# Optimization experiments

Hardware: AMD Instinct MI355X
Metric: run time of the kernel (lower is better)

## Reference

```python
import jax, jax.numpy as jnp
import numpy as np

B, S, I, H, C = 512, 128, 64, 256, 10


def setup_inputs() -> dict:
    key = jax.random.key(0)
    ks = jax.random.split(key, 9)
    u = lambda k, shape, lo, hi: jax.random.uniform(k, shape, jnp.float32, lo, hi)
    return {
        "x": jax.random.normal(ks[0], (B, S, I), jnp.float32),
        # LTCCell params (uniform init per init_parameters)
        "W_gd": u(ks[1], (2 * H, I + H), -0.1, 0.1),
        "b_gd": u(ks[2], (2 * H,), -0.1, 0.1),
        "W_tau": u(ks[3], (H, H), -0.1, 0.1),
        "b_tau": u(ks[4], (H,), -0.1, 0.1),
        "gleak": u(ks[5], (H,), 0.001, 1.0),
        "cm": u(ks[6], (H,), 0.4, 0.6),
        # classifier head
        "W_fc": jax.random.normal(ks[7], (C, H), jnp.float32) * 0.05,
        "b_fc": jax.random.normal(ks[8], (C,), jnp.float32) * 0.05,
    }


def reference(x, W_gd, b_gd, W_tau, b_tau, gleak, cm, W_fc, b_fc):
    # Constant part of the denominator (elementwise, hidden_dim)
    const_den = jax.nn.softplus(cm) + jax.nn.softplus(gleak)  # [H]

    def dhdt(h, x_t):
        # LTCCell.forward: dh/dt
        combined = jnp.concatenate([x_t, h], axis=1)          # [B, I+H]
        gd = combined @ W_gd.T + b_gd                          # [B, 2H]
        gate, dyn = jnp.split(gd, 2, axis=1)
        tau = jax.nn.softplus(h @ W_tau.T + b_tau)             # [B, H]
        num = jax.nn.sigmoid(gate) * jnp.tanh(dyn) - h
        return num / (tau + const_den + 1e-6)

    def step(h, x_t):
        # torchdiffeq 'rk4' fixed-grid = 3/8-rule RK4, single step dt=1 over [0,1]
        k1 = dhdt(h, x_t)
        k2 = dhdt(h + k1 / 3.0, x_t)
        k3 = dhdt(h + (k2 - k1 / 3.0), x_t)
        k4 = dhdt(h + (k1 - k2 + k3), x_t)
        h_new = h + (k1 + 3.0 * (k2 + k3) + k4) * 0.125
        return h_new, None

    h0 = jnp.zeros((x.shape[0], H), x.dtype)
    xs = jnp.transpose(x, (1, 0, 2))                           # [S, B, I]
    h_final, _ = jax.lax.scan(step, h0, xs)
    return h_final @ W_fc.T + b_fc                             # [B, C]
```

## Files before the change

kernel.cpp:

```cpp
#include <hip/hip_runtime.h>

typedef __attribute__((ext_vector_type(8))) short bf16x8;
typedef __attribute__((ext_vector_type(4))) float f32x4;
typedef __attribute__((ext_vector_type(2))) _Float16 f16x2;

#define MFMA(a, b, c) __builtin_amdgcn_mfma_f32_16x16x32_bf16((a), (b), (c), 0, 0, 0)

__device__ __forceinline__ unsigned short f2bf(float f) {
    unsigned int u = __builtin_bit_cast(unsigned int, f);
    return (unsigned short)((u + 0x7FFFu + ((u >> 16) & 1u)) >> 16);
}

__global__ __launch_bounds__(256) void prepack_kernel(const float* __restrict__ W_gd,
                                                      unsigned short* __restrict__ ws) {
    int i = blockIdx.x * 256 + threadIdx.x;
    ws[i] = f2bf(W_gd[(256 + (i >> 8)) * 320 + 64 + (i & 255)]);
    if (i < 32768) ws[65536 + i] = f2bf(W_gd[(i >> 6) * 320 + (i & 63)]);
}

__global__ __launch_bounds__(512, 1)
void ltc_kernel(
    const float* __restrict__ x, const float* __restrict__ W_gd,
    const float* __restrict__ b_gd, const float* __restrict__ W_tau,
    const float* __restrict__ b_tau, const float* __restrict__ gleak,
    const float* __restrict__ cm, const float* __restrict__ W_fc,
    const float* __restrict__ b_fc, const unsigned short* __restrict__ ws,
    float* __restrict__ out)
{
    const int tid  = threadIdx.x;
    const int lane = tid & 63;
    const int wv   = tid >> 6;
    const int c16  = lane & 15;
    const int kg   = lane >> 4;
    const int row0 = blockIdx.x * 2;

    __shared__ __align__(16) unsigned short tauL[65536];
    __shared__ __align__(16) unsigned short dynL[8192];
    __shared__ __align__(16) unsigned short abuf[2][264];
    __shared__ __align__(16) unsigned short xbuf[2][72];
    __shared__ float hout[2][257];

    const int uA = 32 * wv + c16;
    const int uB = uA + 16;
    const int swzA = (uA & 7) << 3;
    const int swzD = (uA & 3) << 3;

    for (int i = tid; i < 65536; i += 512) {
        int u = i >> 8, k = i & 255;
        tauL[u * 256 + (k ^ ((u & 7) << 3))] = f2bf(W_tau[u * 256 + k]);
    }
    for (int i = tid; i < 8192; i += 512) {
        int u = i >> 5, k = i & 31;
        dynL[u * 32 + (k ^ ((u & 3) << 3))] = f2bf(W_gd[(256 + u) * 320 + 64 + k]);
    }
    for (int i = tid; i < 2 * 264; i += 512) ((unsigned short*)abuf)[i] = 0;

    bf16x8 Wg[2][8];
    {
        const int wrow[2] = { uA, uB };
        #pragma unroll
        for (int t = 0; t < 2; ++t) {
            const float* src = W_gd + wrow[t] * 320 + 64;
            #pragma unroll
            for (int s = 0; s < 8; ++s) {
                const float4* p = (const float4*)(src + s * 32 + kg * 8);
                float4 a = p[0], b = p[1];
                bf16x8 v;
                v[0] = (short)f2bf(a.x); v[1] = (short)f2bf(a.y);
                v[2] = (short)f2bf(a.z); v[3] = (short)f2bf(a.w);
                v[4] = (short)f2bf(b.x); v[5] = (short)f2bf(b.y);
                v[6] = (short)f2bf(b.z); v[7] = (short)f2bf(b.w);
                Wg[t][s] = v;
            }
        }
    }

    const float btau0 = b_tau[uA], btau1 = b_tau[uB];
    const float cden0 = __logf(1.f + __expf(cm[uA])) + __logf(1.f + __expf(gleak[uA])) + 1e-6f;
    const float cden1 = __logf(1.f + __expf(cm[uB])) + __logf(1.f + __expf(gleak[uB])) + 1e-6f;
    float bgd[4] = { b_gd[uA], b_gd[uB], b_gd[256 + uA], b_gd[256 + uB] };

    const int rsel = (c16 < 2) ? c16 : 0;
    const unsigned short* aptr = &abuf[rsel][kg * 8];
    const unsigned short* xptr = &xbuf[rsel][kg * 8];
    const unsigned short* wsx  = ws + 65536;

    float hv[2][2] = {{0.f, 0.f}, {0.f, 0.f}};
    f16x2 zh; zh[0] = (_Float16)0.f; zh[1] = (_Float16)0.f;
    f16x2 kk1[2] = { zh, zh }, kk2[2] = { zh, zh }, kk3[2] = { zh, zh };

    __syncthreads();

    #pragma unroll 1
    for (int ts = 0; ts < 128; ++ts) {
        if (tid < 128) {
            int r = tid >> 6, i = tid & 63;
            xbuf[r][i] = f2bf(x[((row0 + r) * 128 + ts) * 64 + i]);
        }
        __syncthreads();

        f32x4 gx[4];
        #pragma unroll
        for (int t = 0; t < 4; ++t) gx[t] = (f32x4){0.f, 0.f, 0.f, 0.f};
        {
            const int xo[4] = { uA, uB, 256 + uA, 256 + uB };
            #pragma unroll
            for (int s = 0; s < 2; ++s) {
                bf16x8 ax = *(const bf16x8*)(xptr + s * 32);
                #pragma unroll
                for (int t = 0; t < 4; ++t) {
                    bf16x8 bx = *(const bf16x8*)(wsx + xo[t] * 64 + s * 32 + kg * 8);
                    gx[t] = MFMA(ax, bx, gx[t]);
                }
            }
        }
        f16x2 gdx[4];
        #pragma unroll
        for (int t = 0; t < 4; ++t) {
            gdx[t][0] = (_Float16)(gx[t][0] + bgd[t]);
            gdx[t][1] = (_Float16)(gx[t][1] + bgd[t]);
        }

        #pragma unroll
        for (int stg = 0; stg < 4; ++stg) {
            f32x4 T0 = {0.f,0.f,0.f,0.f}, T1 = {0.f,0.f,0.f,0.f};
            f32x4 G0 = {0.f,0.f,0.f,0.f}, G1 = {0.f,0.f,0.f,0.f};
            #pragma unroll
            for (int s = 0; s < 8; ++s) {
                bf16x8 A  = *(const bf16x8*)(aptr + s * 32);
                bf16x8 tA = *(const bf16x8*)(tauL + uA * 256 + ((s * 32 + kg * 8) ^ swzA));
                bf16x8 tB = *(const bf16x8*)(tauL + uB * 256 + ((s * 32 + kg * 8) ^ swzA));
                T0 = MFMA(A, tA, T0);
                T1 = MFMA(A, tB, T1);
                G0 = MFMA(A, Wg[0][s], G0);
                G1 = MFMA(A, Wg[1][s], G1);
            }
            float den[2][2];
            den[0][0] = __logf(1.f + __expf(T0[0] + btau0)) + cden0;
            den[0][1] = __logf(1.f + __expf(T0[1] + btau0)) + cden0;
            den[1][0] = __logf(1.f + __expf(T1[0] + btau1)) + cden1;
            den[1][1] = __logf(1.f + __expf(T1[1] + btau1)) + cden1;

            f32x4 D0 = {0.f,0.f,0.f,0.f};
            {
                bf16x8 A0 = *(const bf16x8*)(aptr);
                bf16x8 dA = *(const bf16x8*)(dynL + uA * 32 + ((kg * 8) ^ swzD));
                D0 = MFMA(A0, dA, D0);
                #pragma unroll
                for (int s = 1; s < 8; ++s) {
                    bf16x8 A = *(const bf16x8*)(aptr + s * 32);
                    bf16x8 B = *(const bf16x8*)(ws + uA * 256 + s * 32 + kg * 8);
                    D0 = MFMA(A, B, D0);
                }
            }
            f32x4 D1 = {0.f,0.f,0.f,0.f};
            {
                bf16x8 A0 = *(const bf16x8*)(aptr);
                bf16x8 dB = *(const bf16x8*)(dynL + uB * 32 + ((kg * 8) ^ swzD));
                D1 = MFMA(A0, dB, D1);
                #pragma unroll
                for (int s = 1; s < 8; ++s) {
                    bf16x8 A = *(const bf16x8*)(aptr + s * 32);
                    bf16x8 B = *(const bf16x8*)(ws + uB * 256 + s * 32 + kg * 8);
                    D1 = MFMA(A, B, D1);
                }
            }
            __syncthreads();

            #pragma unroll
            for (int ti = 0; ti < 2; ++ti) {
                #pragma unroll
                for (int r = 0; r < 2; ++r) {
                    float gate = (ti == 0 ? G0[r] : G1[r]) + (float)gdx[ti][r];
                    float dyn  = (ti == 0 ? D0[r] : D1[r]) + (float)gdx[2 + ti][r];
                    float sig = __fdividef(1.f, 1.f + __expf(-gate));
                    float th  = 1.f - __fdividef(2.f, __expf(2.f * dyn) + 1.f);
                    float k1v = (float)kk1[ti][r];
                    float k2v = (float)kk2[ti][r];
                    float k3v = (float)kk3[ti][r];
                    float h0 = hv[ti][r];
                    float ec;
                    if      (stg == 0) ec = h0;
                    else if (stg == 1) ec = h0 + k1v * (1.f / 3.f);
                    else if (stg == 2) ec = h0 - k1v * (1.f / 3.f) + k2v;
                    else               ec = h0 + k1v - k2v + k3v;
                    float kv = __fdividef(sig * th - ec, den[ti][r]);
                    float en;
                    if (stg == 0)      { kk1[ti][r] = (_Float16)kv; en = h0 + kv * (1.f / 3.f); }
                    else if (stg == 1) { kk2[ti][r] = (_Float16)kv; en = h0 - k1v * (1.f / 3.f) + kv; }
                    else if (stg == 2) { kk3[ti][r] = (_Float16)kv; en = h0 + k1v - k2v + kv; }
                    else               { en = h0 + 0.125f * (k1v + 3.f * (k2v + k3v) + kv); hv[ti][r] = en; }
                    if (lane < 16) {
                        int u = (ti == 0) ? uA : uB;
                        abuf[r][u] = f2bf(en);
                    }
                }
            }
            __syncthreads();
        }
    }

    if (lane < 16) {
        hout[0][uA] = hv[0][0]; hout[1][uA] = hv[0][1];
        hout[0][uB] = hv[1][0]; hout[1][uB] = hv[1][1];
    }
    __syncthreads();
    if (tid < 20) {
        int r = tid / 10, c = tid % 10;
        float acc = b_fc[c];
        for (int k = 0; k < 256; ++k) acc = fmaf(hout[r][k], W_fc[c * 256 + k], acc);
        out[(row0 + r) * 10 + c] = acc;
    }
}

extern "C" void kernel_launch(void* const* d_in, const int* in_sizes, int n_in,
                              void* d_out, int out_size, void* d_ws, size_t ws_size,
                              hipStream_t stream) {
    (void)in_sizes; (void)n_in; (void)out_size; (void)ws_size;
    unsigned short* ws16 = (unsigned short*)d_ws;
    prepack_kernel<<<256, 256, 0, stream>>>((const float*)d_in[1], ws16);
    ltc_kernel<<<256, 512, 0, stream>>>(
        (const float*)d_in[0], (const float*)d_in[1], (const float*)d_in[2],
        (const float*)d_in[3], (const float*)d_in[4], (const float*)d_in[5],
        (const float*)d_in[6], (const float*)d_in[7], (const float*)d_in[8],
        ws16, (float*)d_out);
}
```

Measured before the change: 1.130 ms.

## Software-pipeline global dyn-weight loads and split per-unit MFMA chains with elementwise overlap

Restructures each RK stage so the tau, gate and dyn MFMA chains for unit A are computed and their elementwise update done before unit B's chains. This lets unit B's matrix work overlap unit A's transcendental math. Global loads of the dyn weights are software-pipelined through a rotating 4-entry register buffer so each load is issued several MFMAs before use. The tau LDS swizzle is widened to 16 rows, and the bias and constant denominators move into shared memory to free registers. The cost is more complex index bookkeeping in the rotating buffer, with possible register pressure or scheduling changes.

```diff
diff --git a/kernel.cpp b/kernel.cpp
--- a/kernel.cpp
+++ b/kernel.cpp
@@ -9,6 +9,9 @@
 __device__ __forceinline__ unsigned short f2bf(float f) {
     unsigned int u = __builtin_bit_cast(unsigned int, f);
     return (unsigned short)((u + 0x7FFFu + ((u >> 16) & 1u)) >> 16);
+}
+__device__ __forceinline__ float softplusf(float v) {
+    return __logf(1.f + __expf(v));
 }
 
 __global__ __launch_bounds__(256) void prepack_kernel(const float* __restrict__ W_gd,
@@ -32,28 +35,42 @@
     const int wv   = tid >> 6;
     const int c16  = lane & 15;
     const int kg   = lane >> 4;
+    const int kg8  = kg * 8;
     const int row0 = blockIdx.x * 2;
 
     __shared__ __align__(16) unsigned short tauL[65536];
     __shared__ __align__(16) unsigned short dynL[8192];
     __shared__ __align__(16) unsigned short abuf[2][264];
     __shared__ __align__(16) unsigned short xbuf[2][72];
+    __shared__ __align__(8)  float tcL[512];
+    __shared__ float bgdL[512];
     __shared__ float hout[2][257];
-
-    const int uA = 32 * wv + c16;
-    const int uB = uA + 16;
-    const int swzA = (uA & 7) << 3;
-    const int swzD = (uA & 3) << 3;
 
     for (int i = tid; i < 65536; i += 512) {
         int u = i >> 8, k = i & 255;
-        tauL[u * 256 + (k ^ ((u & 7) << 3))] = f2bf(W_tau[u * 256 + k]);
+        tauL[u * 256 + (k ^ ((u & 15) << 3))] = f2bf(W_tau[i]);
     }
     for (int i = tid; i < 8192; i += 512) {
         int u = i >> 5, k = i & 31;
         dynL[u * 32 + (k ^ ((u & 3) << 3))] = f2bf(W_gd[(256 + u) * 320 + 64 + k]);
     }
     for (int i = tid; i < 2 * 264; i += 512) ((unsigned short*)abuf)[i] = 0;
+    if (tid < 256) {
+        tcL[2 * tid]     = b_tau[tid];
+        tcL[2 * tid + 1] = softplusf(cm[tid]) + softplusf(gleak[tid]) + 1e-6f;
+    }
+    bgdL[tid] = b_gd[tid];
+
+    const int uA = 32 * wv + c16;
+    const int uB = uA + 16;
+    const int tswz = c16 << 3;
+    const unsigned short* tAb = tauL + uA * 256;
+    const unsigned short* tBb = tauL + uB * 256;
+    const bf16x8* dA0p = (const bf16x8*)(dynL + uA * 32 + (kg8 ^ ((c16 & 3) << 3)));
+    const bf16x8* dB0p = (const bf16x8*)(dynL + uB * 32 + (kg8 ^ ((c16 & 3) << 3)));
+    const unsigned short* sA  = ws + uA * 256 + kg8;
+    const unsigned short* sB  = ws + uB * 256 + kg8;
+    const unsigned short* wsx = ws + 65536;
 
     bf16x8 Wg[2][8];
     {
@@ -63,7 +80,7 @@
             const float* src = W_gd + wrow[t] * 320 + 64;
             #pragma unroll
             for (int s = 0; s < 8; ++s) {
-                const float4* p = (const float4*)(src + s * 32 + kg * 8);
+                const float4* p = (const float4*)(src + s * 32 + kg8);
                 float4 a = p[0], b = p[1];
                 bf16x8 v;
                 v[0] = (short)f2bf(a.x); v[1] = (short)f2bf(a.y);
@@ -75,21 +92,42 @@
         }
     }
 
-    const float btau0 = b_tau[uA], btau1 = b_tau[uB];
-    const float cden0 = __logf(1.f + __expf(cm[uA])) + __logf(1.f + __expf(gleak[uA])) + 1e-6f;
-    const float cden1 = __logf(1.f + __expf(cm[uB])) + __logf(1.f + __expf(gleak[uB])) + 1e-6f;
-    float bgd[4] = { b_gd[uA], b_gd[uB], b_gd[256 + uA], b_gd[256 + uB] };
-
     const int rsel = (c16 < 2) ? c16 : 0;
-    const unsigned short* aptr = &abuf[rsel][kg * 8];
-    const unsigned short* xptr = &xbuf[rsel][kg * 8];
-    const unsigned short* wsx  = ws + 65536;
+    const unsigned short* aptr = &abuf[rsel][kg8];
+    const unsigned short* xptr = &xbuf[rsel][kg8];
 
     float hv[2][2] = {{0.f, 0.f}, {0.f, 0.f}};
     f16x2 zh; zh[0] = (_Float16)0.f; zh[1] = (_Float16)0.f;
     f16x2 kk1[2] = { zh, zh }, kk2[2] = { zh, zh }, kk3[2] = { zh, zh };
 
+    bf16x8 pipe[4];
+    pipe[0] = *(const bf16x8*)(sA + 32);
+    pipe[1] = *(const bf16x8*)(sA + 64);
+    pipe[2] = *(const bf16x8*)(sA + 96);
+    pipe[3] = *(const bf16x8*)(sA + 128);
+
     __syncthreads();
+
+#define ELEM(ti, G, D, den, en)                                                  \
+    _Pragma("unroll")                                                            \
+    for (int r = 0; r < 2; ++r) {                                                \
+        float gate = G[r] + (float)gdx[ti][r];                                   \
+        float dyn  = D[r] + (float)gdx[2 + ti][r];                               \
+        float sig = __fdividef(1.f, 1.f + __expf(-gate));                        \
+        float th  = 1.f - __fdividef(2.f, __expf(2.f * dyn) + 1.f);              \
+        float k1v = (float)kk1[ti][r], k2v = (float)kk2[ti][r], k3v = (float)kk3[ti][r]; \
+        float h0 = hv[ti][r];                                                    \
+        float ec;                                                                \
+        if      (stg == 0) ec = h0;                                              \
+        else if (stg == 1) ec = h0 + k1v * (1.f / 3.f);                          \
+        else if (stg == 2) ec = h0 - k1v * (1.f / 3.f) + k2v;                    \
+        else               ec = h0 + k1v - k2v + k3v;                            \
+        float kv = __fdividef(sig * th - ec, den[r]);                            \
+        if (stg == 0)      { kk1[ti][r] = (_Float16)kv; en[r] = h0 + kv * (1.f / 3.f); } \
+        else if (stg == 1) { kk2[ti][r] = (_Float16)kv; en[r] = h0 - k1v * (1.f / 3.f) + kv; } \
+        else if (stg == 2) { kk3[ti][r] = (_Float16)kv; en[r] = h0 + k1v - k2v + kv; } \
+        else               { en[r] = h0 + 0.125f * (k1v + 3.f * (k2v + k3v) + kv); hv[ti][r] = en[r]; } \
+    }
 
     #pragma unroll 1
     for (int ts = 0; ts < 128; ++ts) {
@@ -99,106 +137,84 @@
         }
         __syncthreads();
 
-        f32x4 gx[4];
+        f32x4 gx0 = {0,0,0,0}, gx1 = {0,0,0,0}, gx2 = {0,0,0,0}, gx3 = {0,0,0,0};
         #pragma unroll
-        for (int t = 0; t < 4; ++t) gx[t] = (f32x4){0.f, 0.f, 0.f, 0.f};
+        for (int s = 0; s < 2; ++s) {
+            bf16x8 ax = *(const bf16x8*)(xptr + s * 32);
+            gx0 = MFMA(ax, *(const bf16x8*)(wsx + uA * 64         + s * 32 + kg8), gx0);
+            gx1 = MFMA(ax, *(const bf16x8*)(wsx + uB * 64         + s * 32 + kg8), gx1);
+            gx2 = MFMA(ax, *(const bf16x8*)(wsx + (256 + uA) * 64 + s * 32 + kg8), gx2);
+            gx3 = MFMA(ax, *(const bf16x8*)(wsx + (256 + uB) * 64 + s * 32 + kg8), gx3);
+        }
+        f16x2 gdx[4];
         {
-            const int xo[4] = { uA, uB, 256 + uA, 256 + uB };
-            #pragma unroll
-            for (int s = 0; s < 2; ++s) {
-                bf16x8 ax = *(const bf16x8*)(xptr + s * 32);
-                #pragma unroll
-                for (int t = 0; t < 4; ++t) {
-                    bf16x8 bx = *(const bf16x8*)(wsx + xo[t] * 64 + s * 32 + kg * 8);
-                    gx[t] = MFMA(ax, bx, gx[t]);
-                }
-            }
-        }
-        f16x2 gdx[4];
-        #pragma unroll
-        for (int t = 0; t < 4; ++t) {
-            gdx[t][0] = (_Float16)(gx[t][0] + bgd[t]);
-            gdx[t][1] = (_Float16)(gx[t][1] + bgd[t]);
+            float bg0 = bgdL[uA], bg1 = bgdL[uB], bg2 = bgdL[256 + uA], bg3 = bgdL[256 + uB];
+            gdx[0][0] = (_Float16)(gx0[0] + bg0); gdx[0][1] = (_Float16)(gx0[1] + bg0);
+            gdx[1][0] = (_Float16)(gx1[0] + bg1); gdx[1][1] = (_Float16)(gx1[1] + bg1);
+            gdx[2][0] = (_Float16)(gx2[0] + bg2); gdx[2][1] = (_Float16)(gx2[1] + bg2);
+            gdx[3][0] = (_Float16)(gx3[0] + bg3); gdx[3][1] = (_Float16)(gx3[1] + bg3);
         }
 
         #pragma unroll
         for (int stg = 0; stg < 4; ++stg) {
-            f32x4 T0 = {0.f,0.f,0.f,0.f}, T1 = {0.f,0.f,0.f,0.f};
-            f32x4 G0 = {0.f,0.f,0.f,0.f}, G1 = {0.f,0.f,0.f,0.f};
+            f32x4 T0 = {0,0,0,0}, G0 = {0,0,0,0}, D0 = {0,0,0,0};
+            {
+                bf16x8 A = *(const bf16x8*)(aptr);
+                T0 = MFMA(A, *(const bf16x8*)(tAb + (kg8 ^ tswz)), T0);
+                G0 = MFMA(A, Wg[0][0], G0);
+                D0 = MFMA(A, *dA0p, D0);
+            }
             #pragma unroll
-            for (int s = 0; s < 8; ++s) {
-                bf16x8 A  = *(const bf16x8*)(aptr + s * 32);
-                bf16x8 tA = *(const bf16x8*)(tauL + uA * 256 + ((s * 32 + kg * 8) ^ swzA));
-                bf16x8 tB = *(const bf16x8*)(tauL + uB * 256 + ((s * 32 + kg * 8) ^ swzA));
-                T0 = MFMA(A, tA, T0);
-                T1 = MFMA(A, tB, T1);
+            for (int s = 1; s < 8; ++s) {
+                bf16x8 A = *(const bf16x8*)(aptr + s * 32);
+                T0 = MFMA(A, *(const bf16x8*)(tAb + ((s * 32 + kg8) ^ tswz)), T0);
                 G0 = MFMA(A, Wg[0][s], G0);
+                D0 = MFMA(A, pipe[(2 * stg + s - 1) & 3], D0);
+                if (s + 3 < 7) pipe[(2 * stg + s + 3) & 3] = *(const bf16x8*)(sA + (s + 4) * 32);
+                else           pipe[(2 * stg + s + 3) & 3] = *(const bf16x8*)(sB + (s - 3) * 32);
+            }
+            float2 tc0 = *(const float2*)(tcL + 2 * uA);
+            float den0[2];
+            den0[0] = softplusf(T0[0] + tc0.x) + tc0.y;
+            den0[1] = softplusf(T0[1] + tc0.x) + tc0.y;
+            float en0[2];
+            ELEM(0, G0, D0, den0, en0);
+
+            f32x4 T1 = {0,0,0,0}, G1 = {0,0,0,0}, D1 = {0,0,0,0};
+            {
+                bf16x8 A = *(const bf16x8*)(aptr);
+                T1 = MFMA(A, *(const bf16x8*)(tBb + (kg8 ^ tswz)), T1);
+                G1 = MFMA(A, Wg[1][0], G1);
+                D1 = MFMA(A, *dB0p, D1);
+            }
+            #pragma unroll
+            for (int s = 1; s < 8; ++s) {
+                bf16x8 A = *(const bf16x8*)(aptr + s * 32);
+                T1 = MFMA(A, *(const bf16x8*)(tBb + ((s * 32 + kg8) ^ tswz)), T1);
                 G1 = MFMA(A, Wg[1][s], G1);
-            }
-            float den[2][2];
-            den[0][0] = __logf(1.f + __expf(T0[0] + btau0)) + cden0;
-            den[0][1] = __logf(1.f + __expf(T0[1] + btau0)) + cden0;
-            den[1][0] = __logf(1.f + __expf(T1[0] + btau1)) + cden1;
-            den[1][1] = __logf(1.f + __expf(T1[1] + btau1)) + cden1;
-
-            f32x4 D0 = {0.f,0.f,0.f,0.f};
-            {
-                bf16x8 A0 = *(const bf16x8*)(aptr);
-                bf16x8 dA = *(const bf16x8*)(dynL + uA * 32 + ((kg * 8) ^ swzD));
-                D0 = MFMA(A0, dA, D0);
-                #pragma unroll
-                for (int s = 1; s < 8; ++s) {
-                    bf16x8 A = *(const bf16x8*)(aptr + s * 32);
-                    bf16x8 B = *(const bf16x8*)(ws + uA * 256 + s * 32 + kg * 8);
-                    D0 = MFMA(A, B, D0);
+                D1 = MFMA(A, pipe[(2 * stg + 6 + s) & 3], D1);
+                if (s <= 3) {
+                    pipe[(2 * stg + 10 + s) & 3] = *(const bf16x8*)(sB + (s + 4) * 32);
+                } else {
+                    pipe[(2 * (stg + 1) + s - 4) & 3] = *(const bf16x8*)(sA + (s - 3) * 32);
                 }
             }
-            f32x4 D1 = {0.f,0.f,0.f,0.f};
-            {
-                bf16x8 A0 = *(const bf16x8*)(aptr);
-                bf16x8 dB = *(const bf16x8*)(dynL + uB * 32 + ((kg * 8) ^ swzD));
-                D1 = MFMA(A0, dB, D1);
-                #pragma unroll
-                for (int s = 1; s < 8; ++s) {
-                    bf16x8 A = *(const bf16x8*)(aptr + s * 32);
-                    bf16x8 B = *(const bf16x8*)(ws + uB * 256 + s * 32 + kg * 8);
-                    D1 = MFMA(A, B, D1);
-                }
-            }
+            float2 tc1 = *(const float2*)(tcL + 2 * uB);
+            float den1[2];
+            den1[0] = softplusf(T1[0] + tc1.x) + tc1.y;
+            den1[1] = softplusf(T1[1] + tc1.x) + tc1.y;
+            float en1[2];
+            ELEM(1, G1, D1, den1, en1);
+
             __syncthreads();
-
-            #pragma unroll
-            for (int ti = 0; ti < 2; ++ti) {
-                #pragma unroll
-                for (int r = 0; r < 2; ++r) {
-                    float gate = (ti == 0 ? G0[r] : G1[r]) + (float)gdx[ti][r];
-                    float dyn  = (ti == 0 ? D0[r] : D1[r]) + (float)gdx[2 + ti][r];
-                    float sig = __fdividef(1.f, 1.f + __expf(-gate));
-                    float th  = 1.f - __fdividef(2.f, __expf(2.f * dyn) + 1.f);
-                    float k1v = (float)kk1[ti][r];
-                    float k2v = (float)kk2[ti][r];
-                    float k3v = (float)kk3[ti][r];
-                    float h0 = hv[ti][r];
-                    float ec;
-                    if      (stg == 0) ec = h0;
-                    else if (stg == 1) ec = h0 + k1v * (1.f / 3.f);
-                    else if (stg == 2) ec = h0 - k1v * (1.f / 3.f) + k2v;
-                    else               ec = h0 + k1v - k2v + k3v;
-                    float kv = __fdividef(sig * th - ec, den[ti][r]);
-                    float en;
-                    if (stg == 0)      { kk1[ti][r] = (_Float16)kv; en = h0 + kv * (1.f / 3.f); }
-                    else if (stg == 1) { kk2[ti][r] = (_Float16)kv; en = h0 - k1v * (1.f / 3.f) + kv; }
-                    else if (stg == 2) { kk3[ti][r] = (_Float16)kv; en = h0 + k1v - k2v + kv; }
-                    else               { en = h0 + 0.125f * (k1v + 3.f * (k2v + k3v) + kv); hv[ti][r] = en; }
-                    if (lane < 16) {
-                        int u = (ti == 0) ? uA : uB;
-                        abuf[r][u] = f2bf(en);
-                    }
-                }
+            if (lane < 16) {
+                abuf[0][uA] = f2bf(en0[0]); abuf[1][uA] = f2bf(en0[1]);
+                abuf[0][uB] = f2bf(en1[0]); abuf[1][uB] = f2bf(en1[1]);
             }
             __syncthreads();
         }
     }
+#undef ELEM
 
     if (lane < 16) {
         hout[0][uA] = hv[0][0]; hout[1][uA] = hv[0][1];
```

After: 1.019 ms. 1.11x faster.
